# Kernel tuning notes

Measured on AMD Instinct MI355X. Metric: run time of the kernel, lower is better.

Reference implementation:

```python
import jax, jax.numpy as jnp
import numpy as np

N_TOKENS = 16384
DIM = 7168
N_EXPERTS = 256
N_GROUPS = 8
TOPK_GROUPS = 4
TOPK = 8
ROUTE_SCALE = 2.5


def setup_inputs() -> dict:
    key = jax.random.key(0)
    k1, k2 = jax.random.split(key)
    x = jax.random.normal(k1, (N_TOKENS, DIM), dtype=jnp.float32)
    # kaiming_uniform_(a=sqrt(5)) -> Uniform(-1/sqrt(fan_in), 1/sqrt(fan_in))
    bound = 1.0 / np.sqrt(DIM)
    weight = jax.random.uniform(k2, (N_EXPERTS, DIM), dtype=jnp.float32,
                                minval=-bound, maxval=bound)
    expert_bias = jnp.zeros((N_EXPERTS,), dtype=jnp.float32)
    return {"x": x, "weight": weight, "expert_bias": expert_bias}


def reference(x, weight, expert_bias):
    n = x.shape[0]
    # linear scoring + sigmoid (score_func == 'sigmoid')
    scores = jax.nn.sigmoid(x @ weight.T)            # [n, E]
    biased = scores + expert_bias                    # [n, E]
    # group-limited routing
    bg = biased.reshape(n, N_GROUPS, -1)             # [n, G, E/G]
    top2, _ = jax.lax.top_k(bg, 2)
    group_scores = top2.sum(axis=-1)                 # [n, G]
    _, top_group_idx = jax.lax.top_k(group_scores, TOPK_GROUPS)  # [n, TOPK_GROUPS]
    keep = jax.nn.one_hot(top_group_idx, N_GROUPS, dtype=jnp.float32).sum(axis=1) > 0  # [n, G]
    masked = jnp.where(keep[:, :, None], bg, -jnp.inf).reshape(n, -1)  # [n, E]
    # final top-k over allowed experts
    _, indices = jax.lax.top_k(masked, TOPK)         # [n, TOPK]
    weights = jnp.take_along_axis(scores, indices, axis=1)
    weights = weights / (weights.sum(axis=-1, keepdims=True) + 1e-20)
    weights = weights * ROUTE_SCALE
    return weights.astype(x.dtype), indices
```

## Files before the change

kernel.cpp:

```cpp
#include <hip/hip_runtime.h>
#include <math.h>

#define MTOK 16384
#define NEXP 256
#define KDIM 7168

#define CAPR 1024
#define KSPLIT 8
#define KCH (KDIM / KSPLIT)
#define TAU 2e-5f

#define NKC 224
#define NSTEP 112

typedef _Float16 f16;
typedef __attribute__((ext_vector_type(8))) f16 f16x8;
typedef __attribute__((ext_vector_type(4))) f16 f16x4;
typedef __attribute__((ext_vector_type(4))) float f32x4;

__device__ __forceinline__ void cvt_hilo4(const float4 a, f16x4* h, f16x4* l) {
    float xs[4] = {a.x, a.y, a.z, a.w};
#pragma unroll
    for (int e = 0; e < 4; ++e) {
        f16 hh = (f16)xs[e];
        (*h)[e] = hh;
        (*l)[e] = (f16)((xs[e] - (float)hh) * 2048.f);
    }
}

__global__ void wconv_k(const float* __restrict__ W, f16* __restrict__ Wfrag,
                        int* __restrict__ count) {
    if (blockIdx.x == 0 && threadIdx.x == 0) *count = 0;
    const int e  = blockIdx.x;
    const int kc = threadIdx.x;
    if (kc >= NKC) return;
    const int nt  = e >> 4;
    const int col = e & 15;
    const float* src = W + (size_t)e * KDIM + kc * 32;
    float x[32];
#pragma unroll
    for (int i = 0; i < 8; ++i) {
        float4 v = *(const float4*)(src + i * 4);
        x[i * 4 + 0] = v.x; x[i * 4 + 1] = v.y; x[i * 4 + 2] = v.z; x[i * 4 + 3] = v.w;
    }
#pragma unroll
    for (int k8 = 0; k8 < 4; ++k8) {
        f16x8 h, l;
#pragma unroll
        for (int j = 0; j < 8; ++j) {
            float xv = x[k8 * 8 + j];
            f16 hh = (f16)xv;
            h[j] = hh;
            l[j] = (f16)((xv - (float)hh) * 2048.f);
        }
        const size_t lanepos = (size_t)(k8 * 16 + col) * 8;
        *(f16x8*)(Wfrag + (((size_t)(0 * 16 + nt) * NKC + kc) << 9) + lanepos) = h;
        *(f16x8*)(Wfrag + (((size_t)(1 * 16 + nt) * NKC + kc) << 9) + lanepos) = l;
    }
}

#define SOFT_BARRIER() do {                                                 \
        asm volatile("s_waitcnt lgkmcnt(0)" ::: "memory");                  \
        __builtin_amdgcn_s_barrier();                                       \
    } while (0)

__launch_bounds__(512, 2)
__global__ void gemm_v12_k(const float* __restrict__ X,
                           const f16* __restrict__ Wfrag,
                           float* __restrict__ S) {
    __shared__ f16 A_lds[2][2][8][128][8];

    const int tid  = threadIdx.x;
    const int lane = tid & 63;
    const int w    = tid >> 6;
    const int wr   = w >> 2;
    const int wc   = w & 3;

    const int id   = blockIdx.x;
    const int xcd  = id & 7;
    const int nb   = xcd >> 2;
    const int mb   = (id >> 3) * 4 + (xcd & 3);
    const int m0 = mb * 128;
    const int n0 = nb * 128;

    const int arow = tid >> 2;
    const int kl   = tid & 3;
    const float* xg = X + (size_t)(m0 + arow) * KDIM + kl * 4;
    const int ghalf = (kl & 1) * 4;
    const int gbase = kl >> 1;

    const int fr = lane & 15;
    const int fq = lane >> 4;

    const int ntb = nb * 8 + wc * 2;
    const f16* wpH0 = Wfrag + (((size_t)(ntb + 0)  * NKC) << 9) + lane * 8;
    const f16* wpH1 = Wfrag + (((size_t)(ntb + 1)  * NKC) << 9) + lane * 8;
    const f16* wpL0 = Wfrag + (((size_t)(ntb + 16) * NKC) << 9) + lane * 8;
    const f16* wpL1 = Wfrag + (((size_t)(ntb + 17) * NKC) << 9) + lane * 8;

    f32x4 accA[4][2];
    f32x4 accB[4][2];
#pragma unroll
    for (int i = 0; i < 4; ++i)
#pragma unroll
        for (int j = 0; j < 2; ++j) { accA[i][j] = (f32x4)0.f; accB[i][j] = (f32x4)0.f; }

    float4 aE0, aE1, aE2, aE3, aO0, aO1, aO2, aO3;
    f16x8 p0, p1, p2, p3, p4, p5, p6, p7;
    f16x8 q0, q1, q2, q3, q4, q5, q6, q7;

#define A_LOAD4(R0_, R1_, R2_, R3_, STEP_) do {                             \
        const int st_ = (STEP_) < NSTEP ? (STEP_) : (NSTEP - 1);            \
        const float* p_ = xg + (size_t)st_ * 64;                            \
        R0_ = *(const float4*)(p_ + 0);                                     \
        R1_ = *(const float4*)(p_ + 16);                                    \
        R2_ = *(const float4*)(p_ + 32);                                    \
        R3_ = *(const float4*)(p_ + 48);                                    \
    } while (0)

#define B_LOAD8(R0_,R1_,R2_,R3_,R4_,R5_,R6_,R7_, STEP_) do {                \
        const int st_ = (STEP_) < NSTEP ? (STEP_) : (NSTEP - 1);            \
        const size_t oa_ = ((size_t)(st_ * 2))     << 9;                    \
        const size_t ob_ = ((size_t)(st_ * 2 + 1)) << 9;                    \
        R0_ = *(const f16x8*)(wpH0 + oa_);                                  \
        R1_ = *(const f16x8*)(wpH1 + oa_);                                  \
        R2_ = *(const f16x8*)(wpL0 + oa_);                                  \
        R3_ = *(const f16x8*)(wpL1 + oa_);                                  \
        R4_ = *(const f16x8*)(wpH0 + ob_);                                  \
        R5_ = *(const f16x8*)(wpH1 + ob_);                                  \
        R6_ = *(const f16x8*)(wpL0 + ob_);                                  \
        R7_ = *(const f16x8*)(wpL1 + ob_);                                  \
    } while (0)

#define ST_HG(BUF_, R_, I_) do {                                            \
        f16x4 h_, l_;                                                       \
        cvt_hilo4(R_, &h_, &l_);                                            \
        *(f16x4*)&A_lds[BUF_][0][gbase + 2 * (I_)][arow][ghalf] = h_;       \
        *(f16x4*)&A_lds[BUF_][1][gbase + 2 * (I_)][arow][ghalf] = l_;       \
    } while (0)

#define STORE_A4(BUF_, R0_, R1_, R2_, R3_) do {                             \
        ST_HG(BUF_, R0_, 0);                                                \
        ST_HG(BUF_, R1_, 1);                                                \
        ST_HG(BUF_, R2_, 2);                                                \
        ST_HG(BUF_, R3_, 3);                                                \
    } while (0)

#define MFMA16(A_, B_, C_) __builtin_amdgcn_mfma_f32_16x16x32_f16(A_, B_, C_, 0, 0, 0)

#define COMPUTE_CH(BUF_, K8O_, H0_, H1_, L0_, L1_) do {                     \
        f16x8 ah_[4], al_[4];                                               \
        _Pragma("unroll")                                                   \
        for (int mi_ = 0; mi_ < 4; ++mi_) {                                 \
            const int r_ = wr * 64 + mi_ * 16 + fr;                         \
            ah_[mi_] = *(const f16x8*)&A_lds[BUF_][0][(K8O_) + fq][r_][0];  \
            al_[mi_] = *(const f16x8*)&A_lds[BUF_][1][(K8O_) + fq][r_][0];  \
        }                                                                   \
        _Pragma("unroll")                                                   \
        for (int mi_ = 0; mi_ < 4; ++mi_) {                                 \
            accA[mi_][0] = MFMA16(ah_[mi_], H0_, accA[mi_][0]);             \
            accA[mi_][1] = MFMA16(ah_[mi_], H1_, accA[mi_][1]);             \
            accB[mi_][0] = MFMA16(ah_[mi_], L0_, accB[mi_][0]);             \
            accB[mi_][0] = MFMA16(al_[mi_], H0_, accB[mi_][0]);             \
            accB[mi_][1] = MFMA16(ah_[mi_], L1_, accB[mi_][1]);             \
            accB[mi_][1] = MFMA16(al_[mi_], H1_, accB[mi_][1]);             \
        }                                                                   \
    } while (0)

    A_LOAD4(aE0, aE1, aE2, aE3, 0);
    A_LOAD4(aO0, aO1, aO2, aO3, 1);
    B_LOAD8(p0, p1, p2, p3, p4, p5, p6, p7, 0);
    STORE_A4(0, aE0, aE1, aE2, aE3);
    SOFT_BARRIER();

    for (int s = 0; s < NSTEP; s += 2) {
        A_LOAD4(aE0, aE1, aE2, aE3, s + 2);
        B_LOAD8(q0, q1, q2, q3, q4, q5, q6, q7, s + 1);
        COMPUTE_CH(0, 0, p0, p1, p2, p3);
        COMPUTE_CH(0, 4, p4, p5, p6, p7);
        STORE_A4(1, aO0, aO1, aO2, aO3);
        SOFT_BARRIER();

        A_LOAD4(aO0, aO1, aO2, aO3, s + 3);
        B_LOAD8(p0, p1, p2, p3, p4, p5, p6, p7, s + 2);
        COMPUTE_CH(1, 0, q0, q1, q2, q3);
        COMPUTE_CH(1, 4, q4, q5, q6, q7);
        STORE_A4(0, aE0, aE1, aE2, aE3);
        SOFT_BARRIER();
    }

#pragma unroll
    for (int mi = 0; mi < 4; ++mi)
#pragma unroll
        for (int ni = 0; ni < 2; ++ni) {
            const int e = n0 + wc * 32 + ni * 16 + fr;
#pragma unroll
            for (int r = 0; r < 4; ++r) {
                const int m = m0 + wr * 64 + mi * 16 + fq * 4 + r;
                float logit = accA[mi][ni][r] + accB[mi][ni][r] * (1.f / 2048.f);
                S[(size_t)m * NEXP + e] = 1.f / (1.f + expf(-logit));
            }
        }
#undef A_LOAD4
#undef B_LOAD8
#undef ST_HG
#undef STORE_A4
#undef MFMA16
#undef COMPUTE_CH
}

__launch_bounds__(256)
__global__ void route_flag_k(const float* __restrict__ S,
                             const float* __restrict__ bias,
                             float* __restrict__ out,
                             int* __restrict__ list,
                             int* __restrict__ count) {
    __shared__ float sraw[4][256];
    const int wv   = threadIdx.x >> 6;
    const int lane = threadIdx.x & 63;
    const int token = blockIdx.x * 4 + wv;
    const float NINF = -__builtin_inff();
    const float PINF =  __builtin_inff();

    const float* row = S + (size_t)token * NEXP;
    float4 v = *(const float4*)(row + lane * 4);
    *(float4*)&sraw[wv][lane * 4] = v;

    const int e0 = lane * 4;
    float4 bi4 = *(const float4*)(bias + e0);
    float b0 = v.x + bi4.x;
    float b1 = v.y + bi4.y;
    float b2 = v.z + bi4.z;
    float b3 = v.w + bi4.w;

    bool flag = false;

    float m1 = b0, m2 = NINF;
    if (b1 > m1) { m2 = m1; m1 = b1; } else if (b1 > m2) m2 = b1;
    if (b2 > m1) { m2 = m1; m1 = b2; } else if (b2 > m2) m2 = b2;
    if (b3 > m1) { m2 = m1; m1 = b3; } else if (b3 > m2) m2 = b3;
#pragma unroll
    for (int w = 1; w <= 4; w <<= 1) {
        float o1 = __shfl_xor(m1, w);
        float o2 = __shfl_xor(m2, w);
        float nm1 = fmaxf(m1, o1);
        float nm2 = fmaxf(fminf(m1, o1), fmaxf(m2, o2));
        m1 = nm1; m2 = nm2;
    }
    const float gs = m1 + m2;
    const int g = lane >> 3;

    int rank = 0;
#pragma unroll
    for (int j = 0; j < 8; ++j) {
        float gj = __shfl(gs, j * 8);
        rank += (gj > gs) || (gj == gs && j < g);
    }
    const bool sel = rank < 4;

    {
        float a = sel ? gs : PINF;
        float b = sel ? NINF : gs;
#pragma unroll
        for (int w = 1; w < 64; w <<= 1) {
            a = fminf(a, __shfl_xor(a, w));
            b = fmaxf(b, __shfl_xor(b, w));
        }
        flag |= (a - b) < 2.f * TAU;
    }

    if (!sel) { b0 = NINF; b1 = NINF; b2 = NINF; b3 = NINF; }

    int myidx = 0;
    float prev = 0.f;
#pragma unroll
    for (int it = 0; it < 9; ++it) {
        float bv = b0; int bi = e0;
        if (b1 > bv) { bv = b1; bi = e0 + 1; }
        if (b2 > bv) { bv = b2; bi = e0 + 2; }
        if (b3 > bv) { bv = b3; bi = e0 + 3; }
#pragma unroll
        for (int w = 1; w < 64; w <<= 1) {
            float ov = __shfl_xor(bv, w);
            int   oi = __shfl_xor(bi, w);
            if (ov > bv || (ov == bv && oi < bi)) { bv = ov; bi = oi; }
        }
        if (it > 0) flag |= (prev - bv) < TAU;
        prev = bv;
        if (it < 8) {
            if (lane == it) myidx = bi;
            if ((bi >> 2) == lane) {
                switch (bi & 3) {
                    case 0: b0 = NINF; break;
                    case 1: b1 = NINF; break;
                    case 2: b2 = NINF; break;
                    case 3: b3 = NINF; break;
                }
            }
        }
    }

    const bool anyflag = __any((int)flag);

    __syncthreads();

    float wval = (lane < 8) ? sraw[wv][myidx] : 0.f;
    float s = wval;
    s += __shfl_xor(s, 1);
    s += __shfl_xor(s, 2);
    s += __shfl_xor(s, 4);
    if (lane < 8) {
        float wout = wval / (s + 1e-20f) * 2.5f;
        out[(size_t)token * 8 + lane] = wout;
        out[(size_t)MTOK * 8 + (size_t)token * 8 + lane] = (float)myidx;
    }

    if (anyflag && lane == 0) {
        int f = atomicAdd(count, 1);
        if (f < CAPR) list[f] = token;
    }
}

__launch_bounds__(256)
__global__ void rescore_k(const float* __restrict__ X,
                          const float* __restrict__ W,
                          const int* __restrict__ list,
                          const int* __restrict__ count,
                          double* __restrict__ Ldp) {
    const int cnt = min(*count, CAPR);
    const int m0 = blockIdx.x * 64;
    if (m0 >= cnt) return;
    const int n0 = blockIdx.y * 64;
    const int ks = blockIdx.z;
    const int kbase = ks * KCH;

    __shared__ float As[16][66];
    __shared__ float Bs[16][66];
    const int tid = threadIdx.x;
    const int row = tid >> 2;
    const int c   = tid & 3;
    const int tm  = tid >> 4;
    const int tn  = tid & 15;

    const int gi = list[min(m0 + row, cnt - 1)];
    const float* xg = X + (size_t)gi * KDIM + c * 4;
    const float* wg = W + (size_t)(n0 + row) * KDIM + c * 4;

    double acc[4][4];
#pragma unroll
    for (int i = 0; i < 4; ++i)
#pragma unroll
        for (int j = 0; j < 4; ++j) acc[i][j] = 0.0;

    for (int k0 = kbase; k0 < kbase + KCH; k0 += 16) {
        float4 a = *(const float4*)(xg + k0);
        float4 b = *(const float4*)(wg + k0);
        __syncthreads();
        As[c * 4 + 0][row] = a.x; As[c * 4 + 1][row] = a.y;
        As[c * 4 + 2][row] = a.z; As[c * 4 + 3][row] = a.w;
        Bs[c * 4 + 0][row] = b.x; Bs[c * 4 + 1][row] = b.y;
        Bs[c * 4 + 2][row] = b.z; Bs[c * 4 + 3][row] = b.w;
        __syncthreads();
#pragma unroll
        for (int k = 0; k < 16; ++k) {
            double ad[4], bd[4];
#pragma unroll
            for (int i = 0; i < 4; ++i) ad[i] = (double)As[k][tm * 4 + i];
#pragma unroll
            for (int j = 0; j < 4; ++j) bd[j] = (double)Bs[k][tn * 4 + j];
#pragma unroll
            for (int i = 0; i < 4; ++i)
#pragma unroll
                for (int j = 0; j < 4; ++j)
                    acc[i][j] = fma(ad[i], bd[j], acc[i][j]);
        }
    }

#pragma unroll
    for (int i = 0; i < 4; ++i) {
        const int r = m0 + tm * 4 + i;
        if (r < cnt) {
#pragma unroll
            for (int j = 0; j < 4; ++j)
                Ldp[((size_t)ks * CAPR + r) * NEXP + n0 + tn * 4 + j] = acc[i][j];
        }
    }
}

__launch_bounds__(64)
__global__ void route_exact_k(const double* __restrict__ Ldp,
                              const float* __restrict__ bias,
                              const int* __restrict__ list,
                              const int* __restrict__ count,
                              float* __restrict__ out) {
    const int cnt = min(*count, CAPR);
    const int f = blockIdx.x;
    if (f >= cnt) return;
    const int lane = threadIdx.x;
    const int token = list[f];
    const double NINF = -__builtin_inf();

    const int e0 = lane * 4;
    double l0 = 0.0, l1 = 0.0, l2 = 0.0, l3 = 0.0;
#pragma unroll
    for (int s = 0; s < KSPLIT; ++s) {
        double4 p = *(const double4*)(Ldp + ((size_t)s * CAPR + f) * NEXP + e0);
        l0 += p.x; l1 += p.y; l2 += p.z; l3 += p.w;
    }

    double s0 = 1.0 / (1.0 + exp(-l0));
    double s1 = 1.0 / (1.0 + exp(-l1));
    double s2 = 1.0 / (1.0 + exp(-l2));
    double s3 = 1.0 / (1.0 + exp(-l3));

    float4 bi4 = *(const float4*)(bias + e0);
    double b0 = s0 + (double)bi4.x;
    double b1 = s1 + (double)bi4.y;
    double b2 = s2 + (double)bi4.z;
    double b3 = s3 + (double)bi4.w;

    double m1 = b0, m2 = NINF;
    if (b1 > m1) { m2 = m1; m1 = b1; } else if (b1 > m2) m2 = b1;
    if (b2 > m1) { m2 = m1; m1 = b2; } else if (b2 > m2) m2 = b2;
    if (b3 > m1) { m2 = m1; m1 = b3; } else if (b3 > m2) m2 = b3;
#pragma unroll
    for (int w = 1; w <= 4; w <<= 1) {
        double o1 = __shfl_xor(m1, w);
        double o2 = __shfl_xor(m2, w);
        double nm1 = fmax(m1, o1);
        double nm2 = fmax(fmin(m1, o1), fmax(m2, o2));
        m1 = nm1; m2 = nm2;
    }
    const double gs = m1 + m2;
    const int g = lane >> 3;

    int rank = 0;
#pragma unroll
    for (int j = 0; j < 8; ++j) {
        double gj = __shfl(gs, j * 8);
        rank += (gj > gs) || (gj == gs && j < g);
    }
    if (rank >= 4) { b0 = NINF; b1 = NINF; b2 = NINF; b3 = NINF; }

    int myidx = 0;
#pragma unroll
    for (int it = 0; it < 8; ++it) {
        double bv = b0; int bi = e0;
        if (b1 > bv) { bv = b1; bi = e0 + 1; }
        if (b2 > bv) { bv = b2; bi = e0 + 2; }
        if (b3 > bv) { bv = b3; bi = e0 + 3; }
#pragma unroll
        for (int w = 1; w < 64; w <<= 1) {
            double ov = __shfl_xor(bv, w);
            int    oi = __shfl_xor(bi, w);
            if (ov > bv || (ov == bv && oi < bi)) { bv = ov; bi = oi; }
        }
        if (lane == it) myidx = bi;
        if ((bi >> 2) == lane) {
            switch (bi & 3) {
                case 0: b0 = NINF; break;
                case 1: b1 = NINF; break;
                case 2: b2 = NINF; break;
                case 3: b3 = NINF; break;
            }
        }
    }

    double g0 = __shfl(s0, myidx >> 2);
    double g1 = __shfl(s1, myidx >> 2);
    double g2 = __shfl(s2, myidx >> 2);
    double g3 = __shfl(s3, myidx >> 2);
    const int ss = myidx & 3;
    double wval = (lane < 8) ? (ss == 0 ? g0 : ss == 1 ? g1 : ss == 2 ? g2 : g3) : 0.0;
    double s = wval;
    s += __shfl_xor(s, 1);
    s += __shfl_xor(s, 2);
    s += __shfl_xor(s, 4);
    if (lane < 8) {
        float wout = (float)(wval / (s + 1e-20) * 2.5);
        out[(size_t)token * 8 + lane] = wout;
        out[(size_t)MTOK * 8 + (size_t)token * 8 + lane] = (float)myidx;
    }
}

extern "C" void kernel_launch(void* const* d_in, const int* in_sizes, int n_in,
                              void* d_out, int out_size, void* d_ws, size_t ws_size,
                              hipStream_t stream) {
    const float* X    = (const float*)d_in[0];
    const float* W    = (const float*)d_in[1];
    const float* bias = (const float*)d_in[2];
    float* out = (float*)d_out;

    float*  Lf    = (float*)d_ws;
    double* Ldp   = (double*)d_ws;
    int*    list  = (int*)((char*)d_ws + 16777216);
    int*    cnt   = (int*)((char*)d_ws + 16777216 + CAPR * 4);
    f16*    Wfrag = (f16*)((char*)d_ws + 16777216 + 65536);

    wconv_k<<<NEXP, 256, 0, stream>>>(W, Wfrag, cnt);

    gemm_v12_k<<<256, 512, 0, stream>>>(X, Wfrag, Lf);

    route_flag_k<<<MTOK / 4, 256, 0, stream>>>(Lf, bias, out, list, cnt);

    dim3 g3(CAPR / 64, NEXP / 64, KSPLIT);
    rescore_k<<<g3, 256, 0, stream>>>(X, W, list, cnt, Ldp);

    route_exact_k<<<CAPR, 64, 0, stream>>>(Ldp, bias, list, cnt, out);
}
```

Baseline: 389.3 us.

## Shrink rescore tiles to 16 rows and restore full syncthreads in GEMM

The fp64 rescore kernel now handles 16 flagged tokens per block instead of 64, with each thread computing a 1x4 output instead of 4x4. This spreads the usually small flagged-token count over more blocks, avoiding the case where a few blocks do all the work. The cost is less register reuse and more weight traffic per token. Separately, the GEMM's custom lgkmcnt-wait-plus-barrier is replaced by a plain __syncthreads, which may add stricter waits.

```diff
diff --git a/kernel.cpp b/kernel.cpp
--- a/kernel.cpp
+++ b/kernel.cpp
@@ -59,13 +59,8 @@
     }
 }
 
-#define SOFT_BARRIER() do {                                                 \
-        asm volatile("s_waitcnt lgkmcnt(0)" ::: "memory");                  \
-        __builtin_amdgcn_s_barrier();                                       \
-    } while (0)
-
 __launch_bounds__(512, 2)
-__global__ void gemm_v12_k(const float* __restrict__ X,
+__global__ void gemm_v10_k(const float* __restrict__ X,
                            const f16* __restrict__ Wfrag,
                            float* __restrict__ S) {
     __shared__ f16 A_lds[2][2][8][128][8];
@@ -171,7 +166,7 @@
     A_LOAD4(aO0, aO1, aO2, aO3, 1);
     B_LOAD8(p0, p1, p2, p3, p4, p5, p6, p7, 0);
     STORE_A4(0, aE0, aE1, aE2, aE3);
-    SOFT_BARRIER();
+    __syncthreads();
 
     for (int s = 0; s < NSTEP; s += 2) {
         A_LOAD4(aE0, aE1, aE2, aE3, s + 2);
@@ -179,14 +174,14 @@
         COMPUTE_CH(0, 0, p0, p1, p2, p3);
         COMPUTE_CH(0, 4, p4, p5, p6, p7);
         STORE_A4(1, aO0, aO1, aO2, aO3);
-        SOFT_BARRIER();
+        __syncthreads();
 
         A_LOAD4(aO0, aO1, aO2, aO3, s + 3);
         B_LOAD8(p0, p1, p2, p3, p4, p5, p6, p7, s + 2);
         COMPUTE_CH(1, 0, q0, q1, q2, q3);
         COMPUTE_CH(1, 4, q4, q5, q6, q7);
         STORE_A4(0, aE0, aE1, aE2, aE3);
-        SOFT_BARRIER();
+        __syncthreads();
     }
 
 #pragma unroll
@@ -328,62 +323,52 @@
                           const int* __restrict__ count,
                           double* __restrict__ Ldp) {
     const int cnt = min(*count, CAPR);
-    const int m0 = blockIdx.x * 64;
+    const int m0 = blockIdx.x * 16;
     if (m0 >= cnt) return;
     const int n0 = blockIdx.y * 64;
     const int ks = blockIdx.z;
     const int kbase = ks * KCH;
 
-    __shared__ float As[16][66];
+    __shared__ float As[16][17];
     __shared__ float Bs[16][66];
     const int tid = threadIdx.x;
-    const int row = tid >> 2;
-    const int c   = tid & 3;
-    const int tm  = tid >> 4;
-    const int tn  = tid & 15;
-
-    const int gi = list[min(m0 + row, cnt - 1)];
-    const float* xg = X + (size_t)gi * KDIM + c * 4;
-    const float* wg = W + (size_t)(n0 + row) * KDIM + c * 4;
-
-    double acc[4][4];
-#pragma unroll
-    for (int i = 0; i < 4; ++i)
-#pragma unroll
-        for (int j = 0; j < 4; ++j) acc[i][j] = 0.0;
+    const int ar = tid >> 4;
+    const int ak = tid & 15;
+    const int brow = tid & 63;
+    const int bc4  = tid >> 6;
+    const int tm = tid >> 4;
+    const int tn = tid & 15;
+
+    const int gi = list[min(m0 + ar, cnt - 1)];
+    const float* xg = X + (size_t)gi * KDIM + ak;
+    const float* wg = W + (size_t)(n0 + brow) * KDIM + bc4 * 4;
+
+    double acc[4];
+#pragma unroll
+    for (int j = 0; j < 4; ++j) acc[j] = 0.0;
 
     for (int k0 = kbase; k0 < kbase + KCH; k0 += 16) {
-        float4 a = *(const float4*)(xg + k0);
+        float  a = *(xg + k0);
         float4 b = *(const float4*)(wg + k0);
         __syncthreads();
-        As[c * 4 + 0][row] = a.x; As[c * 4 + 1][row] = a.y;
-        As[c * 4 + 2][row] = a.z; As[c * 4 + 3][row] = a.w;
-        Bs[c * 4 + 0][row] = b.x; Bs[c * 4 + 1][row] = b.y;
-        Bs[c * 4 + 2][row] = b.z; Bs[c * 4 + 3][row] = b.w;
+        As[ak][ar] = a;
+        Bs[bc4 * 4 + 0][brow] = b.x; Bs[bc4 * 4 + 1][brow] = b.y;
+        Bs[bc4 * 4 + 2][brow] = b.z; Bs[bc4 * 4 + 3][brow] = b.w;
         __syncthreads();
 #pragma unroll
         for (int k = 0; k < 16; ++k) {
-            double ad[4], bd[4];
-#pragma unroll
-            for (int i = 0; i < 4; ++i) ad[i] = (double)As[k][tm * 4 + i];
-#pragma unroll
-            for (int j = 0; j < 4; ++j) bd[j] = (double)Bs[k][tn * 4 + j];
-#pragma unroll
-            for (int i = 0; i < 4; ++i)
-#pragma unroll
-                for (int j = 0; j < 4; ++j)
-                    acc[i][j] = fma(ad[i], bd[j], acc[i][j]);
-        }
-    }
-
-#pragma unroll
-    for (int i = 0; i < 4; ++i) {
-        const int r = m0 + tm * 4 + i;
-        if (r < cnt) {
+            double ad = (double)As[k][tm];
 #pragma unroll
             for (int j = 0; j < 4; ++j)
-                Ldp[((size_t)ks * CAPR + r) * NEXP + n0 + tn * 4 + j] = acc[i][j];
-        }
+                acc[j] = fma(ad, (double)Bs[k][tn * 4 + j], acc[j]);
+        }
+    }
+
+    const int r = m0 + tm;
+    if (r < cnt) {
+#pragma unroll
+        for (int j = 0; j < 4; ++j)
+            Ldp[((size_t)ks * CAPR + r) * NEXP + n0 + tn * 4 + j] = acc[j];
     }
 }
 
@@ -499,11 +484,11 @@
 
     wconv_k<<<NEXP, 256, 0, stream>>>(W, Wfrag, cnt);
 
-    gemm_v12_k<<<256, 512, 0, stream>>>(X, Wfrag, Lf);
+    gemm_v10_k<<<256, 512, 0, stream>>>(X, Wfrag, Lf);
 
     route_flag_k<<<MTOK / 4, 256, 0, stream>>>(Lf, bias, out, list, cnt);
 
-    dim3 g3(CAPR / 64, NEXP / 64, KSPLIT);
+    dim3 g3(CAPR / 16, NEXP / 64, KSPLIT);
     rescore_k<<<g3, 256, 0, stream>>>(X, W, list, cnt, Ldp);
 
     route_exact_k<<<CAPR, 64, 0, stream>>>(Ldp, bias, list, cnt, out);
```

After: 420.9 us. 8.1% more time.

## Halve GEMM block to 4 waves with 64x64 per-wave tiles

Applied to the files above, without the earlier changes.

The split-fp16 GEMM block goes from 8 waves to 4, and each wave now computes a 64x64 output tile (4x4 MFMA tiles) instead of 64x32, so every A fragment read from LDS is reused across twice as many B columns. Each thread now loads and converts two rows of A per step, and B is loaded per k-chunk just before use instead of being double-buffered a step ahead. The soft barrier is replaced by __syncthreads. This aims to cut LDS traffic per MFMA, in exchange for more accumulator registers, fewer waves to hide latency, and B loads that are exposed.

```diff
diff --git a/kernel.cpp b/kernel.cpp
--- a/kernel.cpp
+++ b/kernel.cpp
@@ -59,13 +59,8 @@
     }
 }
 
-#define SOFT_BARRIER() do {                                                 \
-        asm volatile("s_waitcnt lgkmcnt(0)" ::: "memory");                  \
-        __builtin_amdgcn_s_barrier();                                       \
-    } while (0)
-
-__launch_bounds__(512, 2)
-__global__ void gemm_v12_k(const float* __restrict__ X,
+__launch_bounds__(256, 2)
+__global__ void gemm_v15_k(const float* __restrict__ X,
                            const f16* __restrict__ Wfrag,
                            float* __restrict__ S) {
     __shared__ f16 A_lds[2][2][8][128][8];
@@ -73,8 +68,8 @@
     const int tid  = threadIdx.x;
     const int lane = tid & 63;
     const int w    = tid >> 6;
-    const int wr   = w >> 2;
-    const int wc   = w & 3;
+    const int wm   = w >> 1;
+    const int wn   = w & 1;
 
     const int id   = blockIdx.x;
     const int xcd  = id & 7;
@@ -92,119 +87,118 @@
     const int fr = lane & 15;
     const int fq = lane >> 4;
 
-    const int ntb = nb * 8 + wc * 2;
+    const int ntb = nb * 8 + wn * 4;
     const f16* wpH0 = Wfrag + (((size_t)(ntb + 0)  * NKC) << 9) + lane * 8;
     const f16* wpH1 = Wfrag + (((size_t)(ntb + 1)  * NKC) << 9) + lane * 8;
+    const f16* wpH2 = Wfrag + (((size_t)(ntb + 2)  * NKC) << 9) + lane * 8;
+    const f16* wpH3 = Wfrag + (((size_t)(ntb + 3)  * NKC) << 9) + lane * 8;
     const f16* wpL0 = Wfrag + (((size_t)(ntb + 16) * NKC) << 9) + lane * 8;
     const f16* wpL1 = Wfrag + (((size_t)(ntb + 17) * NKC) << 9) + lane * 8;
-
-    f32x4 accA[4][2];
-    f32x4 accB[4][2];
+    const f16* wpL2 = Wfrag + (((size_t)(ntb + 18) * NKC) << 9) + lane * 8;
+    const f16* wpL3 = Wfrag + (((size_t)(ntb + 19) * NKC) << 9) + lane * 8;
+
+    f32x4 accA[4][4];
+    f32x4 accB[4][4];
 #pragma unroll
     for (int i = 0; i < 4; ++i)
 #pragma unroll
-        for (int j = 0; j < 2; ++j) { accA[i][j] = (f32x4)0.f; accB[i][j] = (f32x4)0.f; }
-
-    float4 aE0, aE1, aE2, aE3, aO0, aO1, aO2, aO3;
-    f16x8 p0, p1, p2, p3, p4, p5, p6, p7;
-    f16x8 q0, q1, q2, q3, q4, q5, q6, q7;
-
-#define A_LOAD4(R0_, R1_, R2_, R3_, STEP_) do {                             \
+        for (int j = 0; j < 4; ++j) { accA[i][j] = (f32x4)0.f; accB[i][j] = (f32x4)0.f; }
+
+    float4 areg[8];
+    f16x8 bh[4], bl[4];
+
+#define A_LOAD(STEP_) do {                                                  \
         const int st_ = (STEP_) < NSTEP ? (STEP_) : (NSTEP - 1);            \
-        const float* p_ = xg + (size_t)st_ * 64;                            \
-        R0_ = *(const float4*)(p_ + 0);                                     \
-        R1_ = *(const float4*)(p_ + 16);                                    \
-        R2_ = *(const float4*)(p_ + 32);                                    \
-        R3_ = *(const float4*)(p_ + 48);                                    \
+        _Pragma("unroll")                                                   \
+        for (int j_ = 0; j_ < 8; ++j_)                                      \
+            areg[j_] = *(const float4*)(xg + (size_t)(arow + (j_ >> 2) * 64) * 0 \
+                        + (size_t)st_ * 64 + (j_ & 3) * 16                  \
+                        + (size_t)((j_ >> 2) * 64) * KDIM);                 \
     } while (0)
 
-#define B_LOAD8(R0_,R1_,R2_,R3_,R4_,R5_,R6_,R7_, STEP_) do {                \
-        const int st_ = (STEP_) < NSTEP ? (STEP_) : (NSTEP - 1);            \
-        const size_t oa_ = ((size_t)(st_ * 2))     << 9;                    \
-        const size_t ob_ = ((size_t)(st_ * 2 + 1)) << 9;                    \
-        R0_ = *(const f16x8*)(wpH0 + oa_);                                  \
-        R1_ = *(const f16x8*)(wpH1 + oa_);                                  \
-        R2_ = *(const f16x8*)(wpL0 + oa_);                                  \
-        R3_ = *(const f16x8*)(wpL1 + oa_);                                  \
-        R4_ = *(const f16x8*)(wpH0 + ob_);                                  \
-        R5_ = *(const f16x8*)(wpH1 + ob_);                                  \
-        R6_ = *(const f16x8*)(wpL0 + ob_);                                  \
-        R7_ = *(const f16x8*)(wpL1 + ob_);                                  \
+#define B_LOAD(KC_) do {                                                    \
+        const size_t o_ = ((size_t)(KC_)) << 9;                             \
+        bh[0] = *(const f16x8*)(wpH0 + o_);                                 \
+        bh[1] = *(const f16x8*)(wpH1 + o_);                                 \
+        bh[2] = *(const f16x8*)(wpH2 + o_);                                 \
+        bh[3] = *(const f16x8*)(wpH3 + o_);                                 \
+        bl[0] = *(const f16x8*)(wpL0 + o_);                                 \
+        bl[1] = *(const f16x8*)(wpL1 + o_);                                 \
+        bl[2] = *(const f16x8*)(wpL2 + o_);                                 \
+        bl[3] = *(const f16x8*)(wpL3 + o_);                                 \
     } while (0)
 
-#define ST_HG(BUF_, R_, I_) do {                                            \
-        f16x4 h_, l_;                                                       \
-        cvt_hilo4(R_, &h_, &l_);                                            \
-        *(f16x4*)&A_lds[BUF_][0][gbase + 2 * (I_)][arow][ghalf] = h_;       \
-        *(f16x4*)&A_lds[BUF_][1][gbase + 2 * (I_)][arow][ghalf] = l_;       \
+#define STORE_A(BUF_) do {                                                  \
+        _Pragma("unroll")                                                   \
+        for (int j_ = 0; j_ < 8; ++j_) {                                    \
+            f16x4 h_, l_;                                                   \
+            cvt_hilo4(areg[j_], &h_, &l_);                                  \
+            const int g_ = gbase + 2 * (j_ & 3);                            \
+            const int r_ = arow + (j_ >> 2) * 64;                           \
+            *(f16x4*)&A_lds[BUF_][0][g_][r_][ghalf] = h_;                   \
+            *(f16x4*)&A_lds[BUF_][1][g_][r_][ghalf] = l_;                   \
+        }                                                                   \
     } while (0)
 
-#define STORE_A4(BUF_, R0_, R1_, R2_, R3_) do {                             \
-        ST_HG(BUF_, R0_, 0);                                                \
-        ST_HG(BUF_, R1_, 1);                                                \
-        ST_HG(BUF_, R2_, 2);                                                \
-        ST_HG(BUF_, R3_, 3);                                                \
-    } while (0)
-
 #define MFMA16(A_, B_, C_) __builtin_amdgcn_mfma_f32_16x16x32_f16(A_, B_, C_, 0, 0, 0)
 
-#define COMPUTE_CH(BUF_, K8O_, H0_, H1_, L0_, L1_) do {                     \
+#define COMPUTE_CH(BUF_, K8O_) do {                                         \
         f16x8 ah_[4], al_[4];                                               \
         _Pragma("unroll")                                                   \
         for (int mi_ = 0; mi_ < 4; ++mi_) {                                 \
-            const int r_ = wr * 64 + mi_ * 16 + fr;                         \
+            const int r_ = wm * 64 + mi_ * 16 + fr;                         \
             ah_[mi_] = *(const f16x8*)&A_lds[BUF_][0][(K8O_) + fq][r_][0];  \
             al_[mi_] = *(const f16x8*)&A_lds[BUF_][1][(K8O_) + fq][r_][0];  \
         }                                                                   \
         _Pragma("unroll")                                                   \
         for (int mi_ = 0; mi_ < 4; ++mi_) {                                 \
-            accA[mi_][0] = MFMA16(ah_[mi_], H0_, accA[mi_][0]);             \
-            accA[mi_][1] = MFMA16(ah_[mi_], H1_, accA[mi_][1]);             \
-            accB[mi_][0] = MFMA16(ah_[mi_], L0_, accB[mi_][0]);             \
-            accB[mi_][0] = MFMA16(al_[mi_], H0_, accB[mi_][0]);             \
-            accB[mi_][1] = MFMA16(ah_[mi_], L1_, accB[mi_][1]);             \
-            accB[mi_][1] = MFMA16(al_[mi_], H1_, accB[mi_][1]);             \
+            _Pragma("unroll")                                               \
+            for (int ni_ = 0; ni_ < 4; ++ni_) {                             \
+                accA[mi_][ni_] = MFMA16(ah_[mi_], bh[ni_], accA[mi_][ni_]); \
+                accB[mi_][ni_] = MFMA16(ah_[mi_], bl[ni_], accB[mi_][ni_]); \
+                accB[mi_][ni_] = MFMA16(al_[mi_], bh[ni_], accB[mi_][ni_]); \
+            }                                                               \
         }                                                                   \
     } while (0)
 
-    A_LOAD4(aE0, aE1, aE2, aE3, 0);
-    A_LOAD4(aO0, aO1, aO2, aO3, 1);
-    B_LOAD8(p0, p1, p2, p3, p4, p5, p6, p7, 0);
-    STORE_A4(0, aE0, aE1, aE2, aE3);
-    SOFT_BARRIER();
+    A_LOAD(0);
+    STORE_A(0);
+    A_LOAD(1);
+    __syncthreads();
 
     for (int s = 0; s < NSTEP; s += 2) {
-        A_LOAD4(aE0, aE1, aE2, aE3, s + 2);
-        B_LOAD8(q0, q1, q2, q3, q4, q5, q6, q7, s + 1);
-        COMPUTE_CH(0, 0, p0, p1, p2, p3);
-        COMPUTE_CH(0, 4, p4, p5, p6, p7);
-        STORE_A4(1, aO0, aO1, aO2, aO3);
-        SOFT_BARRIER();
-
-        A_LOAD4(aO0, aO1, aO2, aO3, s + 3);
-        B_LOAD8(p0, p1, p2, p3, p4, p5, p6, p7, s + 2);
-        COMPUTE_CH(1, 0, q0, q1, q2, q3);
-        COMPUTE_CH(1, 4, q4, q5, q6, q7);
-        STORE_A4(0, aE0, aE1, aE2, aE3);
-        SOFT_BARRIER();
+        B_LOAD(s * 2);
+        COMPUTE_CH(0, 0);
+        B_LOAD(s * 2 + 1);
+        COMPUTE_CH(0, 4);
+        STORE_A(1);
+        A_LOAD(s + 2);
+        __syncthreads();
+
+        B_LOAD((s + 1) * 2);
+        COMPUTE_CH(1, 0);
+        B_LOAD((s + 1) * 2 + 1);
+        COMPUTE_CH(1, 4);
+        STORE_A(0);
+        A_LOAD(s + 3);
+        __syncthreads();
     }
 
 #pragma unroll
     for (int mi = 0; mi < 4; ++mi)
 #pragma unroll
-        for (int ni = 0; ni < 2; ++ni) {
-            const int e = n0 + wc * 32 + ni * 16 + fr;
+        for (int ni = 0; ni < 4; ++ni) {
+            const int e = n0 + wn * 64 + ni * 16 + fr;
 #pragma unroll
             for (int r = 0; r < 4; ++r) {
-                const int m = m0 + wr * 64 + mi * 16 + fq * 4 + r;
+                const int m = m0 + wm * 64 + mi * 16 + fq * 4 + r;
                 float logit = accA[mi][ni][r] + accB[mi][ni][r] * (1.f / 2048.f);
                 S[(size_t)m * NEXP + e] = 1.f / (1.f + expf(-logit));
             }
         }
-#undef A_LOAD4
-#undef B_LOAD8
-#undef ST_HG
-#undef STORE_A4
+#undef A_LOAD
+#undef B_LOAD
+#undef STORE_A
 #undef MFMA16
 #undef COMPUTE_CH
 }
@@ -499,7 +493,7 @@
 
     wconv_k<<<NEXP, 256, 0, stream>>>(W, Wfrag, cnt);
 
-    gemm_v12_k<<<256, 512, 0, stream>>>(X, Wfrag, Lf);
+    gemm_v15_k<<<256, 256, 0, stream>>>(X, Wfrag, Lf);
 
     route_flag_k<<<MTOK / 4, 256, 0, stream>>>(Lf, bias, out, list, cnt);
 
```

New measurement: 641.5 us. 1.65x slower.
